# Optimization experiments

Hardware: AMD Instinct MI355X
Metric: run time of the kernel (lower is better)

Reference implementation:

```python
import jax, jax.numpy as jnp
import numpy as np


def setup_inputs() -> dict:
    key = jax.random.key(0)
    k1, k2, k3 = jax.random.split(key, 3)
    B, H, W, Cin, Cout = 8, 256, 256, 8, 8
    Fh, Fw = 2 * H - 1, 2 * W - 1  # SAME padding, unit strides -> kernel size 2k-1
    inputs = jax.random.normal(k1, (B, H, W, Cin), dtype=jnp.float32)
    # Kernel is parameterized directly in Fourier space; leading axis 2 = (real, imag).
    kernel = jax.random.normal(k2, (2, Fh, Fw, Cin, Cout), dtype=jnp.float32) * 0.01
    bias = jax.random.normal(k3, (Cout,), dtype=jnp.float32) * 0.01
    return {"inputs": inputs, "kernel": kernel, "bias": bias}


def reference(inputs, kernel, bias):
    # inputs: (B, H, W, Cin); kernel: (2, 2H-1, 2W-1, Cin, Cout); bias: (Cout,)
    B, H, W, Cin = inputs.shape
    Fh, Fw = 2 * H - 1, 2 * W - 1
    complex_kernel = jax.lax.complex(kernel[0], kernel[1])  # (Fh, Fw, Cin, Cout)
    # Zero-pad spatial dims to (2H-1, 2W-1) and FFT (s= pads at the end, same as jnp.pad).
    xf = jnp.fft.fftn(inputs, s=(Fh, Fw), axes=(1, 2))  # (B, Fh, Fw, Cin) complex
    # Contract over in_features in frequency space (linearity of IFFT makes this
    # mathematically identical to ifft-then-sum of the original, but avoids the
    # huge (B, Fh, Fw, Cin, Cout) intermediate).
    yf = jnp.einsum("bhwi,hwio->bhwo", xf, complex_kernel)
    y = jnp.fft.ifftn(yf, axes=(1, 2)).real  # (B, Fh, Fw, Cout)
    # SAME crop: centered slice of size (H, W).
    sh = (Fh - H) // 2
    sw = (Fw - W) // 2
    y = y[:, sh:sh + H, sw:sw + W, :]
    return y + bias
```

## Files before the change

### kernel.cpp

```cpp
#include <hip/hip_runtime.h>

#define TPB 256


typedef _Float16 half8  __attribute__((ext_vector_type(8)));
typedef float    floatx16 __attribute__((ext_vector_type(16)));
typedef unsigned int uintx4 __attribute__((ext_vector_type(4)));

__device__ __forceinline__ void split16(float v, _Float16& h, _Float16& l) {
    h = (_Float16)v;
    l = (_Float16)(v - (float)h);
}

__global__ __launch_bounds__(TPB)
void build_tables_k(_Float16* __restrict__ At, _Float16* __restrict__ Ct,
                    _Float16* __restrict__ C2) {
    int idx = blockIdx.x * TPB + threadIdx.x;
    const float w = (float)(6.28318530717958647692 / 511.0);
    _Float16* T; int R, kc2, K; int mode;
    if (idx < 16384)      { T = At; R = idx >> 5;  kc2 = idx & 31; K = 256; mode = 0; }
    else if (idx < 32768) { int id = idx - 16384; T = Ct; R = id >> 6; kc2 = id & 63; K = 512; mode = 1; }
    else                  { int id = idx - 32768; T = C2; R = id >> 5; kc2 = id & 31; K = 256; mode = 2; }

    half8 vrh, vrl, vih, vil;
    #pragma unroll
    for (int j = 0; j < 8; j++) {
        int k = kc2 * 8 + j;
        float cr = 0.f, ci = 0.f;
        if (mode == 0) {
            if (R < 511) {
                int m = (R * k) % 511;
                float s, c; sincosf(w * (float)m, &s, &c);
                cr = c; ci = -s;
            }
        } else {
            if (!(mode == 1 && k == 511)) {
                int m = (k * (R + 127)) % 511;
                float s, c; sincosf(w * (float)m, &s, &c);
                cr = c; ci = s;
            }
        }
        _Float16 th, tl;
        split16(cr, th, tl); vrh[j] = th; vrl[j] = tl;
        split16(ci, th, tl); vih[j] = th; vil[j] = tl;
    }
    int tile = R >> 5, kcblk = kc2 >> 1, lane = (R & 31) + 32 * (kc2 & 1);
    size_t base = ((size_t)(tile * (K >> 4) + kcblk) * 4) * 512 + lane * 8;
    *(half8*)(T + base)        = vrh;
    *(half8*)(T + base + 512)  = vrl;
    *(half8*)(T + base + 1024) = vih;
    *(half8*)(T + base + 1536) = vil;
}

__global__ __launch_bounds__(TPB)
void txp_k(const float* __restrict__ x, _Float16* __restrict__ xT) {
    __shared__ _Float16 L[8][2][32][40];
    const int tid = threadIdx.x;
    const int b = blockIdx.z, n0 = blockIdx.y * 32, w0 = blockIdx.x * 32;
    #pragma unroll
    for (int pp = 0; pp < 4; pp++) {
        int w = tid & 31, n = pp * 8 + (tid >> 5);
        const float4* src = (const float4*)(x + ((size_t)((b * 256 + n0 + n) * 256) + w0 + w) * 8);
        float4 v0 = src[0], v1 = src[1];
        float vv[8] = {v0.x, v0.y, v0.z, v0.w, v1.x, v1.y, v1.z, v1.w};
        #pragma unroll
        for (int ch = 0; ch < 8; ch++) {
            _Float16 h, lo; split16(vv[ch], h, lo);
            L[ch][0][w][n] = h;
            L[ch][1][w][n] = lo;
        }
    }
    __syncthreads();
    #pragma unroll
    for (int t = 0; t < 8; t++) {
        int c = tid + t * 256;
        int p = c & 1, cc = (c >> 1) & 3, w = (c >> 3) & 31, ch = c >> 8;
        uintx4 v = *(const uintx4*)&L[ch][p][w][cc * 8];
        size_t off = ((size_t)(b * 8 + ch)) * 131072 + (size_t)(w0 + w) * 512
                   + (size_t)((n0 >> 3) + cc) * 16 + p * 8;
        *(uintx4*)(xT + off) = v;
    }
}

__global__ __launch_bounds__(TPB)
void ksym_k(const float* __restrict__ Kr, const float* __restrict__ Ki,
            float* __restrict__ KeR, float* __restrict__ KeI) {
    __shared__ float LR[64][65];
    __shared__ float LI[64][65];
    const int tid = threadIdx.x;
    const int k2  = blockIdx.x >> 3;
    const int k1g = (blockIdx.x & 7) * 64;
    const int k2m = (k2 == 0) ? 0 : 511 - k2;
    const float sc = (k2 == 0) ? 0.5f : 1.0f;
    #pragma unroll
    for (int t = 0; t < 4; t++) {
        int idx = tid + t * 256;
        int j = idx & 15, k1l = idx >> 4;
        int k1 = k1g + k1l;
        float4 rs = {0,0,0,0}, rm = {0,0,0,0}, is = {0,0,0,0}, im = {0,0,0,0};
        if (k1 < 511) {
            int k1m = (k1 == 0) ? 0 : 511 - k1;
            size_t so = ((size_t)(k1  * 511 + k2 )) * 64 + j * 4;
            size_t mo = ((size_t)(k1m * 511 + k2m)) * 64 + j * 4;
            rs = *(const float4*)(Kr + so);
            rm = *(const float4*)(Kr + mo);
            is = *(const float4*)(Ki + so);
            im = *(const float4*)(Ki + mo);
        }
        LR[j*4+0][k1l] = sc * (rs.x + rm.x);
        LR[j*4+1][k1l] = sc * (rs.y + rm.y);
        LR[j*4+2][k1l] = sc * (rs.z + rm.z);
        LR[j*4+3][k1l] = sc * (rs.w + rm.w);
        LI[j*4+0][k1l] = sc * (is.x - im.x);
        LI[j*4+1][k1l] = sc * (is.y - im.y);
        LI[j*4+2][k1l] = sc * (is.z - im.z);
        LI[j*4+3][k1l] = sc * (is.w - im.w);
    }
    __syncthreads();
    const size_t ob = (size_t)k2 * 512 + k1g;
    #pragma unroll
    for (int t = 0; t < 4; t++) {
        int idx = tid + t * 256;
        int io = idx >> 4, fq = idx & 15;
        float4 vr = make_float4(LR[io][fq*4], LR[io][fq*4+1], LR[io][fq*4+2], LR[io][fq*4+3]);
        float4 vi = make_float4(LI[io][fq*4], LI[io][fq*4+1], LI[io][fq*4+2], LI[io][fq*4+3]);
        *(float4*)(KeR + (size_t)io * 131072 + ob + fq * 4) = vr;
        *(float4*)(KeI + (size_t)io * 131072 + ob + fq * 4) = vi;
    }
}

template<int NPD, bool TBA, bool DREAL>
__global__ __launch_bounds__(TPB, 3)
void mgemm_k(int K, const _Float16* __restrict__ Tf,
             const _Float16* __restrict__ Dd, long sDz,
             _Float16* __restrict__ Out, long sOz, int OutKc,
             float* __restrict__ Of, long sOfz, int OfN)
{
    constexpr int SLOTS = NPD * 2;
    constexpr int DE  = TBA ? 64 : 128;
    constexpr int DT  = TBA ? 1 : 2;
    constexpr int TT  = TBA ? 2 : 1;
    constexpr int CPT = DE * SLOTS / TPB;
    constexpr int BUF = DE * SLOTS * 8;
    __shared__ _Float16 sm[2 * BUF];

    const int tid = threadIdx.x;
    const int bm = blockIdx.y * 128, bn = blockIdx.x * 64;
    const int z = blockIdx.z;
    const _Float16* D = Dd + (size_t)z * sDz;

    const int l  = tid & 63;
    const int wv = tid >> 6;
    const int lr = l & 31, lg = l >> 5;
    const int wm = (wv >> 1) * 64, wn = (wv & 1) * 32;
    const int Kc16 = K >> 4;

    const int tb = (TBA ? bm + wm : bn + wn);
    int tTB[TT];
    #pragma unroll
    for (int t = 0; t < TT; t++) tTB[t] = ((tb + t * 32) >> 5) * Kc16;

    const int db = (TBA ? wn : wm);
    int dOff[DT][NPD];
    #pragma unroll
    for (int t = 0; t < DT; t++) {
        int cl = db + t * 32 + lr;
        int sw = cl & (SLOTS - 1);
        #pragma unroll
        for (int p = 0; p < NPD; p++)
            dOff[t][p] = cl * (NPD * 16) + (((p * 2 + lg) ^ sw) * 8);
    }

    const int bSide = (TBA ? bn : bm);
    const _Float16* gP[CPT];
    int lO[CPT];
    #pragma unroll
    for (int j = 0; j < CPT; j++) {
        int cid = tid + j * TPB;
        int col = cid / SLOTS;
        int inner = cid & (SLOTS - 1);
        int p = inner & (NPD - 1);
        int h = inner / NPD;
        gP[j] = D + ((size_t)(bSide + col) * (K >> 3) + h) * (NPD * 8) + p * 8;
        lO[j] = col * (NPD * 16) + (((p * 2 + h) ^ (col & (SLOTS - 1))) * 8);
    }

    floatx16 accR[2], accI[2];
    #pragma unroll
    for (int i = 0; i < 2; i++)
        #pragma unroll
        for (int r = 0; r < 16; r++) { accR[i][r] = 0.f; accI[i][r] = 0.f; }

    uintx4 st[CPT];
    #pragma unroll
    for (int j = 0; j < CPT; j++) { st[j] = *(const uintx4*)gP[j]; gP[j] += NPD * 16; }
    #pragma unroll
    for (int j = 0; j < CPT; j++) *(uintx4*)(sm + lO[j]) = st[j];
    #pragma unroll
    for (int j = 0; j < CPT; j++) { st[j] = *(const uintx4*)gP[j]; gP[j] += NPD * 16; }
    __syncthreads();

    const int NT = K >> 4;
    for (int t = 0; t < NT; t++) {
        const int cur = t & 1;
        const _Float16* smc = sm + cur * BUF;

        half8 tf[TT][4];
        #pragma unroll
        for (int tt = 0; tt < TT; tt++)
            #pragma unroll
            for (int p = 0; p < 4; p++)
                tf[tt][p] = *(const half8*)(Tf + ((size_t)(tTB[tt] + t) * 4 + p) * 512 + l * 8);
        half8 df[DT][NPD];
        #pragma unroll
        for (int dt = 0; dt < DT; dt++)
            #pragma unroll
            for (int p = 0; p < NPD; p++)
                df[dt][p] = *(const half8*)(smc + dOff[dt][p]);

        if constexpr (TBA && NPD == 4 && !DREAL) {
            half8 na[2][2];
            #pragma unroll
            for (int mt = 0; mt < 2; mt++)
                #pragma unroll
                for (int p = 0; p < 2; p++) {
                    uintx4 u = __builtin_bit_cast(uintx4, tf[mt][2 + p]);
                    u ^= 0x80008000u;
                    na[mt][p] = __builtin_bit_cast(half8, u);
                }
            #pragma unroll
            for (int mt = 0; mt < 2; mt++) {
                accR[mt] = __builtin_amdgcn_mfma_f32_32x32x16_f16(tf[mt][0], df[0][0], accR[mt], 0,0,0);
                accR[mt] = __builtin_amdgcn_mfma_f32_32x32x16_f16(tf[mt][0], df[0][1], accR[mt], 0,0,0);
                accR[mt] = __builtin_amdgcn_mfma_f32_32x32x16_f16(tf[mt][1], df[0][0], accR[mt], 0,0,0);
                accR[mt] = __builtin_amdgcn_mfma_f32_32x32x16_f16(na[mt][0], df[0][2], accR[mt], 0,0,0);
                accR[mt] = __builtin_amdgcn_mfma_f32_32x32x16_f16(na[mt][0], df[0][3], accR[mt], 0,0,0);
                accR[mt] = __builtin_amdgcn_mfma_f32_32x32x16_f16(na[mt][1], df[0][2], accR[mt], 0,0,0);
                accI[mt] = __builtin_amdgcn_mfma_f32_32x32x16_f16(tf[mt][0], df[0][2], accI[mt], 0,0,0);
                accI[mt] = __builtin_amdgcn_mfma_f32_32x32x16_f16(tf[mt][0], df[0][3], accI[mt], 0,0,0);
                accI[mt] = __builtin_amdgcn_mfma_f32_32x32x16_f16(tf[mt][1], df[0][2], accI[mt], 0,0,0);
                accI[mt] = __builtin_amdgcn_mfma_f32_32x32x16_f16(tf[mt][2], df[0][0], accI[mt], 0,0,0);
                accI[mt] = __builtin_amdgcn_mfma_f32_32x32x16_f16(tf[mt][2], df[0][1], accI[mt], 0,0,0);
                accI[mt] = __builtin_amdgcn_mfma_f32_32x32x16_f16(tf[mt][3], df[0][0], accI[mt], 0,0,0);
            }
        } else if constexpr (TBA && NPD == 2) {
            #pragma unroll
            for (int mt = 0; mt < 2; mt++) {
                accR[mt] = __builtin_amdgcn_mfma_f32_32x32x16_f16(tf[mt][0], df[0][0], accR[mt], 0,0,0);
                accR[mt] = __builtin_amdgcn_mfma_f32_32x32x16_f16(tf[mt][0], df[0][1], accR[mt], 0,0,0);
                accR[mt] = __builtin_amdgcn_mfma_f32_32x32x16_f16(tf[mt][1], df[0][0], accR[mt], 0,0,0);
                accI[mt] = __builtin_amdgcn_mfma_f32_32x32x16_f16(tf[mt][2], df[0][0], accI[mt], 0,0,0);
                accI[mt] = __builtin_amdgcn_mfma_f32_32x32x16_f16(tf[mt][2], df[0][1], accI[mt], 0,0,0);
                accI[mt] = __builtin_amdgcn_mfma_f32_32x32x16_f16(tf[mt][3], df[0][0], accI[mt], 0,0,0);
            }
        } else {
            half8 nd[2][2];
            #pragma unroll
            for (int mt = 0; mt < 2; mt++)
                #pragma unroll
                for (int p = 0; p < 2; p++) {
                    uintx4 u = __builtin_bit_cast(uintx4, df[mt][2 + p]);
                    u ^= 0x80008000u;
                    nd[mt][p] = __builtin_bit_cast(half8, u);
                }
            #pragma unroll
            for (int mt = 0; mt < 2; mt++) {
                accR[mt] = __builtin_amdgcn_mfma_f32_32x32x16_f16(df[mt][0], tf[0][0], accR[mt], 0,0,0);
                accR[mt] = __builtin_amdgcn_mfma_f32_32x32x16_f16(df[mt][0], tf[0][1], accR[mt], 0,0,0);
                accR[mt] = __builtin_amdgcn_mfma_f32_32x32x16_f16(df[mt][1], tf[0][0], accR[mt], 0,0,0);
                accR[mt] = __builtin_amdgcn_mfma_f32_32x32x16_f16(nd[mt][0], tf[0][2], accR[mt], 0,0,0);
                accR[mt] = __builtin_amdgcn_mfma_f32_32x32x16_f16(nd[mt][0], tf[0][3], accR[mt], 0,0,0);
                accR[mt] = __builtin_amdgcn_mfma_f32_32x32x16_f16(nd[mt][1], tf[0][2], accR[mt], 0,0,0);
            }
        }

        if (t + 1 < NT) {
            _Float16* smn = sm + (cur ^ 1) * BUF;
            #pragma unroll
            for (int j = 0; j < CPT; j++) *(uintx4*)(smn + lO[j]) = st[j];
            if (t + 2 < NT) {
                #pragma unroll
                for (int j = 0; j < CPT; j++) { st[j] = *(const uintx4*)gP[j]; gP[j] += NPD * 16; }
            }
            __syncthreads();
        }
    }

    if constexpr (DREAL) {
        float* Dv = Of + (size_t)z * sOfz;
        #pragma unroll
        for (int mt = 0; mt < 2; mt++)
            #pragma unroll
            for (int r = 0; r < 16; r++) {
                int row = bm + wm + mt * 32 + (r & 3) + 8 * (r >> 2) + 4 * lg;
                int col = bn + wn + lr;
                Dv[(size_t)row * OfN + col] = accR[mt][r];
            }
    } else {
        _Float16* O = Out + (size_t)z * sOz;
        #pragma unroll
        for (int mt = 0; mt < 2; mt++)
            #pragma unroll
            for (int r = 0; r < 16; r++) {
                int row = bm + wm + mt * 32 + (r & 3) + 8 * (r >> 2) + 4 * lg;
                int col = bn + wn + lr;
                size_t base = ((size_t)row * OutKc + (col >> 3)) * 32 + (col & 7);
                _Float16 h, lo;
                split16(accR[mt][r], h, lo);
                O[base]      = h;
                O[base + 8]  = lo;
                split16(accI[mt][r], h, lo);
                O[base + 16] = h;
                O[base + 24] = lo;
            }
    }
}

__global__ __launch_bounds__(TPB)
void einsum_k(_Float16* __restrict__ F, const float* __restrict__ KeR,
              const float* __restrict__ KeI, int g)
{
    const int pt = blockIdx.x * TPB + threadIdx.x;
    const int k2 = pt >> 9, k1 = pt & 511;
    const size_t fo = ((size_t)(k2 * 64 + (k1 >> 3))) * 32 + (k1 & 7);

    for (int b0 = 0; b0 < g; b0 += 4) {
        const int bt = (g - b0 < 4) ? (g - b0) : 4;
        float xr[4][8], xi[4][8];
        #pragma unroll
        for (int bb = 0; bb < 4; bb++) {
            if (bb >= bt) break;
            #pragma unroll
            for (int i = 0; i < 8; i++) {
                const _Float16* P = F + ((size_t)((b0 + bb) * 8 + i)) * 524288 + fo;
                xr[bb][i] = (float)P[0]  + (float)P[8];
                xi[bb][i] = (float)P[16] + (float)P[24];
            }
        }
        #pragma unroll
        for (int o = 0; o < 8; o++) {
            float ar[4] = {0.f,0.f,0.f,0.f}, ai[4] = {0.f,0.f,0.f,0.f};
            #pragma unroll
            for (int i = 0; i < 8; i++) {
                float kr = KeR[(size_t)(i * 8 + o) * 131072 + pt];
                float ki = KeI[(size_t)(i * 8 + o) * 131072 + pt];
                #pragma unroll
                for (int bb = 0; bb < 4; bb++) {
                    ar[bb] = fmaf(xr[bb][i], kr, ar[bb]);
                    ar[bb] = fmaf(-xi[bb][i], ki, ar[bb]);
                    ai[bb] = fmaf(xr[bb][i], ki, ai[bb]);
                    ai[bb] = fmaf(xi[bb][i], kr, ai[bb]);
                }
            }
            #pragma unroll
            for (int bb = 0; bb < 4; bb++) {
                if (bb >= bt) break;
                _Float16* Q = F + ((size_t)((b0 + bb) * 8 + o)) * 524288 + fo;
                _Float16 h, lo;
                split16(ar[bb], h, lo); Q[0]  = h; Q[8]  = lo;
                split16(ai[bb], h, lo); Q[16] = h; Q[24] = lo;
            }
        }
    }
}

__global__ __launch_bounds__(TPB)
void tout_k(const float* __restrict__ Dq, const float* __restrict__ bias,
            float* __restrict__ out, int b0)
{
    int idx = blockIdx.x * TPB + threadIdx.x;
    int o = idx & 7, q = (idx >> 3) & 255, p = (idx >> 11) & 255, bl = idx >> 19;
    float v = Dq[(size_t)(bl * 8 + o) * 65536 + p * 256 + q];
    out[(size_t)(b0 + bl) * 524288 + (size_t)(idx & 524287)] = v * (1.f / 261121.f) + bias[o];
}


extern "C" void kernel_launch(void* const* d_in, const int* in_sizes, int n_in,
                              void* d_out, int out_size, void* d_ws, size_t ws_size,
                              hipStream_t stream) {
    const float* x    = (const float*)d_in[0];
    const float* Kr   = (const float*)d_in[1];
    const float* Ki   = Kr + 16711744;
    const float* bias = (const float*)d_in[2];
    float* out = (float*)d_out;
    char* ws = (char*)d_ws;

    _Float16* AtabF = (_Float16*)(ws + 0);
    _Float16* CtabF = (_Float16*)(ws + 1048576);
    _Float16* Ct2F  = (_Float16*)(ws + 2097152);
    _Float16* xTp   = (_Float16*)(ws + 2621440);
    float*    KeR   = (float*)   (ws + 19398656);
    float*    KeI   = (float*)   (ws + 52953088);
    const size_t fixedEnd = 86507520;

    int g = 1;
    for (int cand = 8; cand >= 1; cand >>= 1) {
        if (fixedEnd + (size_t)cand * 16777216 <= ws_size) { g = cand; break; }
    }
    _Float16* F1  = (_Float16*)(ws + fixedEnd);
    _Float16* F2T = (_Float16*)(ws + fixedEnd + (size_t)g * 8388608);
    _Float16* F1b = F1;
    float*    Dq  = (float*)F2T;

    build_tables_k<<<160, TPB, 0, stream>>>(AtabF, CtabF, Ct2F);
    txp_k<<<dim3(8, 8, 8), TPB, 0, stream>>>(x, xTp);
    ksym_k<<<2048, TPB, 0, stream>>>(Kr, Ki, KeR, KeI);

    for (int b0 = 0; b0 < 8; b0 += g) {
        int Z = g * 8;
        mgemm_k<2, true, false><<<dim3(4, 4, Z), TPB, 0, stream>>>(
            256, AtabF,
            xTp + (size_t)b0 * 8 * 131072, 131072,
            F1, 524288, 32, nullptr, 0, 0);

        mgemm_k<4, true, false><<<dim3(8, 2, Z), TPB, 0, stream>>>(
            256, AtabF,
            F1, 524288,
            F2T, 524288, 64, nullptr, 0, 0);

        einsum_k<<<512, TPB, 0, stream>>>(F2T, KeR, KeI, g);

        mgemm_k<4, true, false><<<dim3(4, 2, Z), TPB, 0, stream>>>(
            512, CtabF,
            F2T, 524288,
            F1b, 262144, 32, nullptr, 0, 0);

        mgemm_k<4, false, true><<<dim3(4, 2, Z), TPB, 0, stream>>>(
            256, Ct2F,
            F1b, 262144,
            nullptr, 0, 0, Dq, 65536, 256);

        tout_k<<<g * 2048, TPB, 0, stream>>>(Dq, bias, out, b0);
    }
}
```

Measured before the change: 506.3 us.

## Parameterize MFMA GEMM warp tiles and prefetch twiddle fragments across iterations

Templates the batched complex GEMM kernel on per-wave tile sizes (WM, WN), so the first two DFT stages use 128x128 block tiles with 64x64 per wave and the later stages get reshaped tiles. The twiddle-table fragments are now loaded one iteration ahead into registers instead of at the top of each k-step, hiding global latency behind the MFMAs. Larger accumulator tiles raise register use, so launch bounds drop from 3 to 2 blocks per CU. Grids shrink, which may reduce occupancy and load balance across CUs.

```diff
diff --git a/kernel.cpp b/kernel.cpp
--- a/kernel.cpp
+++ b/kernel.cpp
@@ -10,6 +10,12 @@
 __device__ __forceinline__ void split16(float v, _Float16& h, _Float16& l) {
     h = (_Float16)v;
     l = (_Float16)(v - (float)h);
+}
+
+__device__ __forceinline__ half8 neg8(half8 v) {
+    uintx4 u = __builtin_bit_cast(uintx4, v);
+    u ^= 0x80008000u;
+    return __builtin_bit_cast(half8, u);
 }
 
 __global__ __launch_bounds__(TPB)
@@ -129,36 +135,38 @@
     }
 }
 
-template<int NPD, bool TBA, bool DREAL>
-__global__ __launch_bounds__(TPB, 3)
+template<int NPD, bool TBA, bool DREAL, int WM, int WN>
+__global__ __launch_bounds__(TPB, 2)
 void mgemm_k(int K, const _Float16* __restrict__ Tf,
              const _Float16* __restrict__ Dd, long sDz,
              _Float16* __restrict__ Out, long sOz, int OutKc,
              float* __restrict__ Of, long sOfz, int OfN)
 {
+    constexpr int MT = WM / 32, NT = WN / 32;
+    constexpr int TT = TBA ? MT : NT;
+    constexpr int DT = TBA ? NT : MT;
     constexpr int SLOTS = NPD * 2;
-    constexpr int DE  = TBA ? 64 : 128;
-    constexpr int DT  = TBA ? 1 : 2;
-    constexpr int TT  = TBA ? 2 : 1;
+    constexpr int DE  = TBA ? 2 * WN : 2 * WM;
     constexpr int CPT = DE * SLOTS / TPB;
     constexpr int BUF = DE * SLOTS * 8;
     __shared__ _Float16 sm[2 * BUF];
 
     const int tid = threadIdx.x;
-    const int bm = blockIdx.y * 128, bn = blockIdx.x * 64;
+    const int bm = blockIdx.y * (2 * WM), bn = blockIdx.x * (2 * WN);
     const int z = blockIdx.z;
     const _Float16* D = Dd + (size_t)z * sDz;
 
     const int l  = tid & 63;
     const int wv = tid >> 6;
     const int lr = l & 31, lg = l >> 5;
-    const int wm = (wv >> 1) * 64, wn = (wv & 1) * 32;
+    const int wm = (wv >> 1) * WM, wn = (wv & 1) * WN;
     const int Kc16 = K >> 4;
 
     const int tb = (TBA ? bm + wm : bn + wn);
-    int tTB[TT];
-    #pragma unroll
-    for (int t = 0; t < TT; t++) tTB[t] = ((tb + t * 32) >> 5) * Kc16;
+    const _Float16* tP[TT];
+    #pragma unroll
+    for (int tt = 0; tt < TT; tt++)
+        tP[tt] = Tf + (size_t)(((tb + tt * 32) >> 5) * Kc16) * 2048 + l * 8;
 
     const int db = (TBA ? wn : wm);
     int dOff[DT][NPD];
@@ -185,11 +193,13 @@
         lO[j] = col * (NPD * 16) + (((p * 2 + h) ^ (col & (SLOTS - 1))) * 8);
     }
 
-    floatx16 accR[2], accI[2];
-    #pragma unroll
-    for (int i = 0; i < 2; i++)
-        #pragma unroll
-        for (int r = 0; r < 16; r++) { accR[i][r] = 0.f; accI[i][r] = 0.f; }
+    floatx16 accR[MT][NT], accI[MT][NT];
+    #pragma unroll
+    for (int i = 0; i < MT; i++)
+        #pragma unroll
+        for (int j = 0; j < NT; j++)
+            #pragma unroll
+            for (int r = 0; r < 16; r++) { accR[i][j][r] = 0.f; accI[i][j][r] = 0.f; }
 
     uintx4 st[CPT];
     #pragma unroll
@@ -198,121 +208,127 @@
     for (int j = 0; j < CPT; j++) *(uintx4*)(sm + lO[j]) = st[j];
     #pragma unroll
     for (int j = 0; j < CPT; j++) { st[j] = *(const uintx4*)gP[j]; gP[j] += NPD * 16; }
+    half8 tf[TT][4];
+    #pragma unroll
+    for (int tt = 0; tt < TT; tt++) {
+        #pragma unroll
+        for (int p = 0; p < 4; p++) tf[tt][p] = *(const half8*)(tP[tt] + p * 512);
+        tP[tt] += 2048;
+    }
     __syncthreads();
 
-    const int NT = K >> 4;
-    for (int t = 0; t < NT; t++) {
-        const int cur = t & 1;
+    const int NTs = K >> 4;
+    int cur = 0;
+    for (int t = 0; t < NTs; t++) {
         const _Float16* smc = sm + cur * BUF;
 
-        half8 tf[TT][4];
-        #pragma unroll
-        for (int tt = 0; tt < TT; tt++)
-            #pragma unroll
-            for (int p = 0; p < 4; p++)
-                tf[tt][p] = *(const half8*)(Tf + ((size_t)(tTB[tt] + t) * 4 + p) * 512 + l * 8);
-        half8 df[DT][NPD];
-        #pragma unroll
-        for (int dt = 0; dt < DT; dt++)
+        half8 na[TT][2];
+        if constexpr (TBA && NPD == 4 && !DREAL) {
+            #pragma unroll
+            for (int tt = 0; tt < TT; tt++) {
+                na[tt][0] = neg8(tf[tt][2]);
+                na[tt][1] = neg8(tf[tt][3]);
+            }
+        }
+
+        #pragma unroll
+        for (int dt = 0; dt < DT; dt++) {
+            half8 dfl[NPD];
             #pragma unroll
             for (int p = 0; p < NPD; p++)
-                df[dt][p] = *(const half8*)(smc + dOff[dt][p]);
-
-        if constexpr (TBA && NPD == 4 && !DREAL) {
-            half8 na[2][2];
-            #pragma unroll
-            for (int mt = 0; mt < 2; mt++)
-                #pragma unroll
-                for (int p = 0; p < 2; p++) {
-                    uintx4 u = __builtin_bit_cast(uintx4, tf[mt][2 + p]);
-                    u ^= 0x80008000u;
-                    na[mt][p] = __builtin_bit_cast(half8, u);
-                }
-            #pragma unroll
-            for (int mt = 0; mt < 2; mt++) {
-                accR[mt] = __builtin_amdgcn_mfma_f32_32x32x16_f16(tf[mt][0], df[0][0], accR[mt], 0,0,0);
-                accR[mt] = __builtin_amdgcn_mfma_f32_32x32x16_f16(tf[mt][0], df[0][1], accR[mt], 0,0,0);
-                accR[mt] = __builtin_amdgcn_mfma_f32_32x32x16_f16(tf[mt][1], df[0][0], accR[mt], 0,0,0);
-                accR[mt] = __builtin_amdgcn_mfma_f32_32x32x16_f16(na[mt][0], df[0][2], accR[mt], 0,0,0);
-                accR[mt] = __builtin_amdgcn_mfma_f32_32x32x16_f16(na[mt][0], df[0][3], accR[mt], 0,0,0);
-                accR[mt] = __builtin_amdgcn_mfma_f32_32x32x16_f16(na[mt][1], df[0][2], accR[mt], 0,0,0);
-                accI[mt] = __builtin_amdgcn_mfma_f32_32x32x16_f16(tf[mt][0], df[0][2], accI[mt], 0,0,0);
-                accI[mt] = __builtin_amdgcn_mfma_f32_32x32x16_f16(tf[mt][0], df[0][3], accI[mt], 0,0,0);
-                accI[mt] = __builtin_amdgcn_mfma_f32_32x32x16_f16(tf[mt][1], df[0][2], accI[mt], 0,0,0);
-                accI[mt] = __builtin_amdgcn_mfma_f32_32x32x16_f16(tf[mt][2], df[0][0], accI[mt], 0,0,0);
-                accI[mt] = __builtin_amdgcn_mfma_f32_32x32x16_f16(tf[mt][2], df[0][1], accI[mt], 0,0,0);
-                accI[mt] = __builtin_amdgcn_mfma_f32_32x32x16_f16(tf[mt][3], df[0][0], accI[mt], 0,0,0);
-            }
-        } else if constexpr (TBA && NPD == 2) {
-            #pragma unroll
-            for (int mt = 0; mt < 2; mt++) {
-                accR[mt] = __builtin_amdgcn_mfma_f32_32x32x16_f16(tf[mt][0], df[0][0], accR[mt], 0,0,0);
-                accR[mt] = __builtin_amdgcn_mfma_f32_32x32x16_f16(tf[mt][0], df[0][1], accR[mt], 0,0,0);
-                accR[mt] = __builtin_amdgcn_mfma_f32_32x32x16_f16(tf[mt][1], df[0][0], accR[mt], 0,0,0);
-                accI[mt] = __builtin_amdgcn_mfma_f32_32x32x16_f16(tf[mt][2], df[0][0], accI[mt], 0,0,0);
-                accI[mt] = __builtin_amdgcn_mfma_f32_32x32x16_f16(tf[mt][2], df[0][1], accI[mt], 0,0,0);
-                accI[mt] = __builtin_amdgcn_mfma_f32_32x32x16_f16(tf[mt][3], df[0][0], accI[mt], 0,0,0);
-            }
-        } else {
-            half8 nd[2][2];
-            #pragma unroll
-            for (int mt = 0; mt < 2; mt++)
-                #pragma unroll
-                for (int p = 0; p < 2; p++) {
-                    uintx4 u = __builtin_bit_cast(uintx4, df[mt][2 + p]);
-                    u ^= 0x80008000u;
-                    nd[mt][p] = __builtin_bit_cast(half8, u);
-                }
-            #pragma unroll
-            for (int mt = 0; mt < 2; mt++) {
-                accR[mt] = __builtin_amdgcn_mfma_f32_32x32x16_f16(df[mt][0], tf[0][0], accR[mt], 0,0,0);
-                accR[mt] = __builtin_amdgcn_mfma_f32_32x32x16_f16(df[mt][0], tf[0][1], accR[mt], 0,0,0);
-                accR[mt] = __builtin_amdgcn_mfma_f32_32x32x16_f16(df[mt][1], tf[0][0], accR[mt], 0,0,0);
-                accR[mt] = __builtin_amdgcn_mfma_f32_32x32x16_f16(nd[mt][0], tf[0][2], accR[mt], 0,0,0);
-                accR[mt] = __builtin_amdgcn_mfma_f32_32x32x16_f16(nd[mt][0], tf[0][3], accR[mt], 0,0,0);
-                accR[mt] = __builtin_amdgcn_mfma_f32_32x32x16_f16(nd[mt][1], tf[0][2], accR[mt], 0,0,0);
-            }
-        }
-
-        if (t + 1 < NT) {
+                dfl[p] = *(const half8*)(smc + dOff[dt][p]);
+
+            if constexpr (TBA && NPD == 4 && !DREAL) {
+                #pragma unroll
+                for (int mt = 0; mt < MT; mt++) {
+                    accR[mt][dt] = __builtin_amdgcn_mfma_f32_32x32x16_f16(tf[mt][0], dfl[0], accR[mt][dt], 0,0,0);
+                    accR[mt][dt] = __builtin_amdgcn_mfma_f32_32x32x16_f16(tf[mt][0], dfl[1], accR[mt][dt], 0,0,0);
+                    accR[mt][dt] = __builtin_amdgcn_mfma_f32_32x32x16_f16(tf[mt][1], dfl[0], accR[mt][dt], 0,0,0);
+                    accR[mt][dt] = __builtin_amdgcn_mfma_f32_32x32x16_f16(na[mt][0], dfl[2], accR[mt][dt], 0,0,0);
+                    accR[mt][dt] = __builtin_amdgcn_mfma_f32_32x32x16_f16(na[mt][0], dfl[3], accR[mt][dt], 0,0,0);
+                    accR[mt][dt] = __builtin_amdgcn_mfma_f32_32x32x16_f16(na[mt][1], dfl[2], accR[mt][dt], 0,0,0);
+                    accI[mt][dt] = __builtin_amdgcn_mfma_f32_32x32x16_f16(tf[mt][0], dfl[2], accI[mt][dt], 0,0,0);
+                    accI[mt][dt] = __builtin_amdgcn_mfma_f32_32x32x16_f16(tf[mt][0], dfl[3], accI[mt][dt], 0,0,0);
+                    accI[mt][dt] = __builtin_amdgcn_mfma_f32_32x32x16_f16(tf[mt][1], dfl[2], accI[mt][dt], 0,0,0);
+                    accI[mt][dt] = __builtin_amdgcn_mfma_f32_32x32x16_f16(tf[mt][2], dfl[0], accI[mt][dt], 0,0,0);
+                    accI[mt][dt] = __builtin_amdgcn_mfma_f32_32x32x16_f16(tf[mt][2], dfl[1], accI[mt][dt], 0,0,0);
+                    accI[mt][dt] = __builtin_amdgcn_mfma_f32_32x32x16_f16(tf[mt][3], dfl[0], accI[mt][dt], 0,0,0);
+                }
+            } else if constexpr (TBA && NPD == 2) {
+                #pragma unroll
+                for (int mt = 0; mt < MT; mt++) {
+                    accR[mt][dt] = __builtin_amdgcn_mfma_f32_32x32x16_f16(tf[mt][0], dfl[0], accR[mt][dt], 0,0,0);
+                    accR[mt][dt] = __builtin_amdgcn_mfma_f32_32x32x16_f16(tf[mt][0], dfl[1], accR[mt][dt], 0,0,0);
+                    accR[mt][dt] = __builtin_amdgcn_mfma_f32_32x32x16_f16(tf[mt][1], dfl[0], accR[mt][dt], 0,0,0);
+                    accI[mt][dt] = __builtin_amdgcn_mfma_f32_32x32x16_f16(tf[mt][2], dfl[0], accI[mt][dt], 0,0,0);
+                    accI[mt][dt] = __builtin_amdgcn_mfma_f32_32x32x16_f16(tf[mt][2], dfl[1], accI[mt][dt], 0,0,0);
+                    accI[mt][dt] = __builtin_amdgcn_mfma_f32_32x32x16_f16(tf[mt][3], dfl[0], accI[mt][dt], 0,0,0);
+                }
+            } else {
+                half8 nd0 = neg8(dfl[2]);
+                half8 nd1 = neg8(dfl[3]);
+                #pragma unroll
+                for (int nt = 0; nt < NT; nt++) {
+                    accR[dt][nt] = __builtin_amdgcn_mfma_f32_32x32x16_f16(dfl[0], tf[nt][0], accR[dt][nt], 0,0,0);
+                    accR[dt][nt] = __builtin_amdgcn_mfma_f32_32x32x16_f16(dfl[0], tf[nt][1], accR[dt][nt], 0,0,0);
+                    accR[dt][nt] = __builtin_amdgcn_mfma_f32_32x32x16_f16(dfl[1], tf[nt][0], accR[dt][nt], 0,0,0);
+                    accR[dt][nt] = __builtin_amdgcn_mfma_f32_32x32x16_f16(nd0, tf[nt][2], accR[dt][nt], 0,0,0);
+                    accR[dt][nt] = __builtin_amdgcn_mfma_f32_32x32x16_f16(nd0, tf[nt][3], accR[dt][nt], 0,0,0);
+                    accR[dt][nt] = __builtin_amdgcn_mfma_f32_32x32x16_f16(nd1, tf[nt][2], accR[dt][nt], 0,0,0);
+                }
+            }
+        }
+
+        if (t + 1 < NTs) {
             _Float16* smn = sm + (cur ^ 1) * BUF;
             #pragma unroll
             for (int j = 0; j < CPT; j++) *(uintx4*)(smn + lO[j]) = st[j];
-            if (t + 2 < NT) {
+            #pragma unroll
+            for (int tt = 0; tt < TT; tt++) {
+                #pragma unroll
+                for (int p = 0; p < 4; p++) tf[tt][p] = *(const half8*)(tP[tt] + p * 512);
+                tP[tt] += 2048;
+            }
+            if (t + 2 < NTs) {
                 #pragma unroll
                 for (int j = 0; j < CPT; j++) { st[j] = *(const uintx4*)gP[j]; gP[j] += NPD * 16; }
             }
-            __syncthreads();
-        }
+        }
+        __syncthreads();
+        cur ^= 1;
     }
 
     if constexpr (DREAL) {
         float* Dv = Of + (size_t)z * sOfz;
         #pragma unroll
-        for (int mt = 0; mt < 2; mt++)
-            #pragma unroll
-            for (int r = 0; r < 16; r++) {
-                int row = bm + wm + mt * 32 + (r & 3) + 8 * (r >> 2) + 4 * lg;
-                int col = bn + wn + lr;
-                Dv[(size_t)row * OfN + col] = accR[mt][r];
-            }
+        for (int mt = 0; mt < MT; mt++)
+            #pragma unroll
+            for (int nt = 0; nt < NT; nt++)
+                #pragma unroll
+                for (int r = 0; r < 16; r++) {
+                    int row = bm + wm + mt * 32 + (r & 3) + 8 * (r >> 2) + 4 * lg;
+                    int col = bn + wn + nt * 32 + lr;
+                    Dv[(size_t)row * OfN + col] = accR[mt][nt][r];
+                }
     } else {
         _Float16* O = Out + (size_t)z * sOz;
         #pragma unroll
-        for (int mt = 0; mt < 2; mt++)
-            #pragma unroll
-            for (int r = 0; r < 16; r++) {
-                int row = bm + wm + mt * 32 + (r & 3) + 8 * (r >> 2) + 4 * lg;
-                int col = bn + wn + lr;
-                size_t base = ((size_t)row * OutKc + (col >> 3)) * 32 + (col & 7);
-                _Float16 h, lo;
-                split16(accR[mt][r], h, lo);
-                O[base]      = h;
-                O[base + 8]  = lo;
-                split16(accI[mt][r], h, lo);
-                O[base + 16] = h;
-                O[base + 24] = lo;
-            }
+        for (int mt = 0; mt < MT; mt++)
+            #pragma unroll
+            for (int nt = 0; nt < NT; nt++)
+                #pragma unroll
+                for (int r = 0; r < 16; r++) {
+                    int row = bm + wm + mt * 32 + (r & 3) + 8 * (r >> 2) + 4 * lg;
+                    int col = bn + wn + nt * 32 + lr;
+                    size_t base = ((size_t)row * OutKc + (col >> 3)) * 32 + (col & 7);
+                    _Float16 h, lo;
+                    split16(accR[mt][nt][r], h, lo);
+                    O[base]      = h;
+                    O[base + 8]  = lo;
+                    split16(accI[mt][nt][r], h, lo);
+                    O[base + 16] = h;
+                    O[base + 24] = lo;
+                }
     }
 }
 
@@ -408,24 +424,24 @@
 
     for (int b0 = 0; b0 < 8; b0 += g) {
         int Z = g * 8;
-        mgemm_k<2, true, false><<<dim3(4, 4, Z), TPB, 0, stream>>>(
+        mgemm_k<2, true, false, 64, 64><<<dim3(2, 4, Z), TPB, 0, stream>>>(
             256, AtabF,
             xTp + (size_t)b0 * 8 * 131072, 131072,
             F1, 524288, 32, nullptr, 0, 0);
 
-        mgemm_k<4, true, false><<<dim3(8, 2, Z), TPB, 0, stream>>>(
+        mgemm_k<4, true, false, 64, 64><<<dim3(4, 2, Z), TPB, 0, stream>>>(
             256, AtabF,
             F1, 524288,
             F2T, 524288, 64, nullptr, 0, 0);
 
         einsum_k<<<512, TPB, 0, stream>>>(F2T, KeR, KeI, g);
 
-        mgemm_k<4, true, false><<<dim3(4, 2, Z), TPB, 0, stream>>>(
+        mgemm_k<4, true, false, 32, 64><<<dim3(2, 4, Z), TPB, 0, stream>>>(
             512, CtabF,
             F2T, 524288,
             F1b, 262144, 32, nullptr, 0, 0);
 
-        mgemm_k<4, false, true><<<dim3(4, 2, Z), TPB, 0, stream>>>(
+        mgemm_k<4, false, true, 64, 32><<<dim3(4, 2, Z), TPB, 0, stream>>>(
             256, Ct2F,
             F1b, 262144,
             nullptr, 0, 0, Dq, 65536, 256);
```

Measured after the change: 475.0 us. 6.2% less time.
